# Kernel optimization log

Measured on AMD Instinct MI355X. Metric: run time of the kernel, lower is better.

The kernel has to match this reference:

```python
import jax, jax.numpy as jnp
import numpy as np

B, F, M, N, H, O = 8, 128, 256, 1024, 64, 128
BN_EPS = 1e-5
COS_EPS = 1e-8


def _bn(x, g, b, m, v):
    # inference-mode BatchNorm over channel axis 1
    shape = [1] * x.ndim
    shape[1] = -1
    return g.reshape(shape) * (x - m.reshape(shape)) * jax.lax.rsqrt(v.reshape(shape) + BN_EPS) + b.reshape(shape)


def setup_inputs() -> dict:
    key = jax.random.key(0)
    ks = jax.random.split(key, 24)
    def n(k, shape, s=1.0):
        return jax.random.normal(k, shape, dtype=jnp.float32) * s
    inp = {}
    inp['template_feature'] = n(ks[0], (B, F, M))
    inp['search_feature'] = n(ks[1], (B, F, N))
    # SharedMLP 1x1 conv weights (bias=False because bn=True)
    inp['W1'] = n(ks[2], (H, F + 1), 0.05)
    inp['W2'] = n(ks[3], (H, H), 0.05)
    inp['W3'] = n(ks[4], (H, H), 0.05)
    # fea_layer: conv1d(H, bn=True) then conv1d(O, activation=None, bias=True)
    inp['Wc1'] = n(ks[5], (H, H), 0.05)
    inp['Wc2'] = n(ks[6], (O, H), 0.05)
    inp['bc2'] = n(ks[7], (O,), 0.05)
    for i, nm in enumerate(['1', '2', '3', 'c1']):
        inp['g' + nm] = 1.0 + n(ks[8 + i], (H,), 0.1)
        inp['b' + nm] = n(ks[12 + i], (H,), 0.1)
        inp['m' + nm] = n(ks[16 + i], (H,), 0.01)
        inp['v' + nm] = jax.random.uniform(ks[20 + i], (H,), minval=0.5, maxval=1.5, dtype=jnp.float32)
    return inp


def reference(template_feature, search_feature, W1, W2, W3, Wc1, Wc2, bc2,
              g1, b1, m1, v1, g2, b2, m2, v2, g3, b3, m3, v3, gc1, bc1, mc1, vc1):
    t, s = template_feature, search_feature
    # pairwise cosine similarity over channel dim (no BxFxMxN expand needed)
    dot = jnp.einsum('bfm,bfn->bmn', t, s)
    nt = jnp.linalg.norm(t, axis=1)  # (B, M)
    ns = jnp.linalg.norm(s, axis=1)  # (B, N)
    cos = dot / jnp.maximum(nt[:, :, None] * ns[:, None, :], COS_EPS)  # (B, M, N)
    # first 1x1 conv on concat(cos, expand(t)) computed fused (no concat materialization)
    h = jnp.einsum('hf,bfm->bhm', W1[:, 1:], t)[..., None] + W1[:, 0][None, :, None, None] * cos[:, None]
    h = jax.nn.relu(_bn(h, g1, b1, m1, v1))  # (B, H, M, N)
    h = jax.nn.relu(_bn(jnp.einsum('gh,bhmn->bgmn', W2, h), g2, b2, m2, v2))
    h = jax.nn.relu(_bn(jnp.einsum('gh,bhmn->bgmn', W3, h), g3, b3, m3, v3))
    p = jnp.max(h, axis=2)  # max-pool over M -> (B, H, N)
    c = jax.nn.relu(_bn(jnp.einsum('gh,bhn->bgn', Wc1, p), gc1, bc1, mc1, vc1))
    return jnp.einsum('oh,bhn->bon', Wc2, c) + bc2[None, :, None]  # (B, O, N)
```

## Files before the change

kernel.cpp:

```cpp
#include <hip/hip_runtime.h>


#define BB 8
#define FF 128
#define MM 256
#define NN 1024
#define HH 64
#define OO 128
#define BN_EPS 1e-5f
#define COS_EPS 1e-8f

#define WS_U     0
#define WS_C2    64
#define WS_C3    128
#define WS_CC1   192
#define WS_W2H   256
#define WS_W3H   2304
#define WS_WC1F  8448
#define WS_A1    12544
#define WS_NT    143616
#define WS_NS    145664
#define WS_COSH  153856
#define WS_P     1202432
#define PS       524288

typedef _Float16 half2v __attribute__((ext_vector_type(2)));
typedef _Float16 half4  __attribute__((ext_vector_type(4)));
typedef _Float16 half8  __attribute__((ext_vector_type(8)));
typedef __attribute__((ext_vector_type(4))) float f32x4;

__device__ __forceinline__ unsigned int pkh2(float a, float b){
  auto h = __builtin_amdgcn_cvt_pkrtz(a, b);
  return __builtin_bit_cast(unsigned int, h);
}
__device__ __forceinline__ half2v u2h(unsigned int u){
  return __builtin_bit_cast(half2v, u);
}
__device__ __forceinline__ unsigned int h2u(half2v v){
  return __builtin_bit_cast(unsigned int, v);
}
__device__ __forceinline__ unsigned int relu2(unsigned int d){
  half2v v = __builtin_elementwise_max(u2h(d), (half2v){(_Float16)0, (_Float16)0});
  return h2u(v);
}
__device__ __forceinline__ unsigned int bh1(unsigned int up, half2v c, unsigned int ap){
  half2v v = __builtin_elementwise_fma(u2h(up), c, u2h(ap));
  v = __builtin_elementwise_max(v, (half2v){(_Float16)0, (_Float16)0});
  return h2u(v);
}
__device__ __forceinline__ float dot4(float4 a, float4 b, float acc){
  acc = fmaf(a.x, b.x, acc); acc = fmaf(a.y, b.y, acc);
  acc = fmaf(a.z, b.z, acc); acc = fmaf(a.w, b.w, acc);
  return acc;
}

__global__ __launch_bounds__(256) void k_prep(const float* t_, const float* s_,
    const float* W1, const float* W2, const float* W3, const float* Wc1,
    const float* g1, const float* b1, const float* m1, const float* v1,
    const float* g2, const float* b2, const float* m2, const float* v2,
    const float* g3, const float* b3, const float* m3, const float* v3,
    const float* gc1,const float* bc1,const float* mc1,const float* vc1,
    float* ws){
  __shared__ float W1s[64][133];
  int t = threadIdx.x;
  int bx = blockIdx.x;
  if (bx < 256){
    int b = bx >> 5, m0 = (bx & 31)*8;
    for (int idx = t; idx < 8192; idx += 256){
      int h = idx >> 7, f = idx & 127;
      W1s[h][f] = W1[h*129 + 1 + f];
    }
    __syncthreads();
    int h = t & 63, mg = t >> 6;
    const float* tp = t_ + (size_t)b*FF*MM + m0 + mg*2;
    float acc0 = 0.f, acc1 = 0.f;
    for (int f = 0; f < FF; f++){
      float wv = W1s[h][f];
      float2 tv = *(const float2*)&tp[(size_t)f*MM];
      acc0 = fmaf(wv, tv.x, acc0); acc1 = fmaf(wv, tv.y, acc1);
    }
    float a1 = g1[h] / sqrtf(v1[h] + BN_EPS);
    float c1 = b1[h] - a1*m1[h];
    unsigned short* dst = (unsigned short*)(ws + WS_A1) + ((size_t)(b*MM + m0 + mg*2))*64 + h;
    dst[0]  = (unsigned short)(pkh2(fmaf(a1, acc0, c1), 0.f) & 0xFFFFu);
    dst[64] = (unsigned short)(pkh2(fmaf(a1, acc1, c1), 0.f) & 0xFFFFu);
  } else if (bx < 416){
    __shared__ float red[4][64];
    int x = t & 63, fq = t >> 6;
    int idx = (bx - 256)*64 + x;
    const float* ptr; size_t stride;
    if (idx < BB*MM){
      int b = idx >> 8, m = idx & 255;
      ptr = t_ + (size_t)b*FF*MM + m; stride = MM;
    } else {
      int j = idx - BB*MM;
      int b = j >> 10, n = j & 1023;
      ptr = s_ + (size_t)b*FF*NN + n; stride = NN;
    }
    float acc = 0.f;
    for (int f = fq*32; f < fq*32 + 32; f++){
      float v = ptr[(size_t)f*stride]; acc = fmaf(v, v, acc);
    }
    red[fq][x] = acc;
    __syncthreads();
    if (fq == 0)
      ws[WS_NT + idx] = sqrtf(red[0][x] + red[1][x] + red[2][x] + red[3][x]);
  } else {
    if (t < 64){
      float a1 = g1[t] / sqrtf(v1[t] + BN_EPS);
      ws[WS_U + t]   = a1 * W1[t*129];
      float a2 = g2[t] / sqrtf(v2[t] + BN_EPS);
      ws[WS_C2 + t]  = b2[t] - a2*m2[t];
      float a3 = g3[t] / sqrtf(v3[t] + BN_EPS);
      ws[WS_C3 + t]  = b3[t] - a3*m3[t];
      float ac = gc1[t] / sqrtf(vc1[t] + BN_EPS);
      ws[WS_CC1 + t] = bc1[t] - ac*mc1[t];
    }
    unsigned short* w2h = (unsigned short*)(ws + WS_W2H);
    unsigned short* w3h = (unsigned short*)(ws + WS_W3H);
    for (int i = t; i < 4096; i += 256){
      int g = i >> 6;
      float a2 = g2[g] / sqrtf(v2[g] + BN_EPS);
      w2h[i] = __builtin_bit_cast(unsigned short, (_Float16)(a2 * W2[i]));
      float a3 = g3[g] / sqrtf(v3[g] + BN_EPS);
      w3h[i] = __builtin_bit_cast(unsigned short, (_Float16)(a3 * W3[i]));
      float ac = gc1[g] / sqrtf(vc1[g] + BN_EPS);
      ws[WS_WC1F + i] = ac * Wc1[i];
    }
  }
}

__global__ __launch_bounds__(256) void k_cos(const float* t_, const float* s_, float* ws){
  __shared__ __align__(16) unsigned short tS[64][136];
  __shared__ __align__(16) unsigned short sS[64][136];
  __shared__ float ntS[64], nsS[64];
  int t = threadIdx.x;
  int lane = t & 63, w = t >> 6;
  int ln15 = lane & 15, quad = lane >> 4;
  int m0 = blockIdx.x*64, n0 = blockIdx.y*64, b = blockIdx.z;
  {
    int x = t & 63;
    const float* tb = t_ + (size_t)b*FF*MM + m0 + x;
    const float* sb = s_ + (size_t)b*FF*NN + n0 + x;
    #pragma unroll
    for (int k = 0; k < 16; k++){
      int fp = w*16 + k;
      *(unsigned int*)&tS[x][2*fp] = pkh2(tb[(size_t)(2*fp)*MM], tb[(size_t)(2*fp+1)*MM]);
      *(unsigned int*)&sS[x][2*fp] = pkh2(sb[(size_t)(2*fp)*NN], sb[(size_t)(2*fp+1)*NN]);
    }
    if (t < 64) ntS[t] = ws[WS_NT + b*MM + m0 + t];
    else if (t < 128) nsS[t-64] = ws[WS_NS + b*NN + n0 + (t-64)];
  }
  __syncthreads();
  half8 A4[4];
  #pragma unroll
  for (int kc = 0; kc < 4; kc++)
    A4[kc] = *(const half8*)&sS[w*16 + ln15][kc*32 + quad*8];
  float4 ns4 = *(const float4*)&nsS[w*16 + quad*4];
  int nb = n0 + w*16 + quad*4;
  unsigned short* cosw = (unsigned short*)(ws + WS_COSH);
  #pragma unroll
  for (int mt = 0; mt < 4; mt++){
    f32x4 acc = (f32x4){0.f,0.f,0.f,0.f};
    #pragma unroll
    for (int kc = 0; kc < 4; kc++){
      half8 B4 = *(const half8*)&tS[mt*16 + ln15][kc*32 + quad*8];
      acc = __builtin_amdgcn_mfma_f32_16x16x32_f16(A4[kc], B4, acc, 0, 0, 0);
    }
    int m = m0 + mt*16 + ln15;
    float ntv = ntS[mt*16 + ln15];
    float c0 = acc[0] * __builtin_amdgcn_rcpf(fmaxf(ntv*ns4.x, COS_EPS));
    float c1 = acc[1] * __builtin_amdgcn_rcpf(fmaxf(ntv*ns4.y, COS_EPS));
    float c2 = acc[2] * __builtin_amdgcn_rcpf(fmaxf(ntv*ns4.z, COS_EPS));
    float c3 = acc[3] * __builtin_amdgcn_rcpf(fmaxf(ntv*ns4.w, COS_EPS));
    uint2 vv;
    vv.x = pkh2(c0, c1);
    vv.y = pkh2(c2, c3);
    *(uint2*)&cosw[(size_t)(b*MM + m)*NN + nb] = vv;
  }
}

__global__ __launch_bounds__(256, 3) void k_main(const float* ws, float* Pp){
  __shared__ __align__(16) float redS[3][16][68];
  int t = threadIdx.x;
  int lane = t & 63, w = t >> 6;
  int ln15 = lane & 15, quad = lane >> 4;
  int b = blockIdx.y;
  int n0 = blockIdx.x * 16;
  int ms = blockIdx.z;

  const unsigned short* w2h = (const unsigned short*)(ws + WS_W2H);
  const unsigned short* w3h = (const unsigned short*)(ws + WS_W3H);
  half8 W2A[4][2];
  half4 W3A[4][4];
  f32x4 c2v[4];
  #pragma unroll
  for (int rt = 0; rt < 4; rt++){
    int g = rt*16 + ln15;
    #pragma unroll
    for (int kk = 0; kk < 2; kk++)
      W2A[rt][kk] = *(const half8*)&w2h[g*64 + kk*32 + quad*8];
    #pragma unroll
    for (int ks = 0; ks < 4; ks++)
      W3A[rt][ks] = *(const half4*)&w3h[g*64 + ks*16 + quad*4];
    float4 cb2 = *(const float4*)&ws[WS_C2 + rt*16 + quad*4];
    c2v[rt] = (f32x4){cb2.x, cb2.y, cb2.z, cb2.w};
  }
  f32x4 zf = (f32x4){0.f, 0.f, 0.f, 0.f};
  unsigned int upk[2][4];
  #pragma unroll
  for (int kk = 0; kk < 2; kk++){
    float4 ua = *(const float4*)&ws[WS_U + kk*32 + quad*8];
    float4 ub = *(const float4*)&ws[WS_U + kk*32 + quad*8 + 4];
    upk[kk][0] = pkh2(ua.x, ua.y); upk[kk][1] = pkh2(ua.z, ua.w);
    upk[kk][2] = pkh2(ub.x, ub.y); upk[kk][3] = pkh2(ub.z, ub.w);
  }
  const unsigned short* A1H = (const unsigned short*)(ws + WS_A1) + (size_t)b*MM*64;
  int n = n0 + ln15;
  const unsigned short* cosP = (const unsigned short*)(ws + WS_COSH)
                               + (size_t)b*MM*NN + n;

  f32x4 p[4];
  #pragma unroll
  for (int rt = 0; rt < 4; rt++)
    p[rt] = (f32x4){-3.0e38f, -3.0e38f, -3.0e38f, -3.0e38f};

  int m0i = ms*128 + w;
  unsigned int cu = cosP[(size_t)m0i*NN];
  uint4 a1a = *(const uint4*)&A1H[(size_t)m0i*64 + quad*8];
  uint4 a1b = *(const uint4*)&A1H[(size_t)m0i*64 + 32 + quad*8];

  for (int mc = 0; mc < 32; mc++){
    int mN = ms*128 + (mc < 31 ? mc + 1 : 31)*4 + w;
    unsigned int cuN = cosP[(size_t)mN*NN];
    uint4 a1aN = *(const uint4*)&A1H[(size_t)mN*64 + quad*8];
    uint4 a1bN = *(const uint4*)&A1H[(size_t)mN*64 + 32 + quad*8];

    unsigned int cd = cu | (cu << 16);
    half2v ch = u2h(cd);
    uint4 q0, q1;
    q0.x = bh1(upk[0][0], ch, a1a.x); q0.y = bh1(upk[0][1], ch, a1a.y);
    q0.z = bh1(upk[0][2], ch, a1a.z); q0.w = bh1(upk[0][3], ch, a1a.w);
    q1.x = bh1(upk[1][0], ch, a1b.x); q1.y = bh1(upk[1][1], ch, a1b.y);
    q1.z = bh1(upk[1][2], ch, a1b.z); q1.w = bh1(upk[1][3], ch, a1b.w);
    half8 b0h = __builtin_bit_cast(half8, q0);
    half8 b1h = __builtin_bit_cast(half8, q1);

    f32x4 acc[4];
    #pragma unroll
    for (int rt = 0; rt < 4; rt++){
      acc[rt] = __builtin_amdgcn_mfma_f32_16x16x32_f16(W2A[rt][0], b0h, c2v[rt], 0, 0, 0);
      acc[rt] = __builtin_amdgcn_mfma_f32_16x16x32_f16(W2A[rt][1], b1h, acc[rt], 0, 0, 0);
    }

    half4 pk[4];
    #pragma unroll
    for (int ks = 0; ks < 4; ks++){
      uint2 vv;
      vv.x = relu2(pkh2(acc[ks][0], acc[ks][1]));
      vv.y = relu2(pkh2(acc[ks][2], acc[ks][3]));
      pk[ks] = __builtin_bit_cast(half4, vv);
    }

    #pragma unroll
    for (int rt = 0; rt < 4; rt++){
      f32x4 a3 = __builtin_amdgcn_mfma_f32_16x16x16f16(W3A[rt][0], pk[0], zf, 0, 0, 0);
      a3 = __builtin_amdgcn_mfma_f32_16x16x16f16(W3A[rt][1], pk[1], a3, 0, 0, 0);
      a3 = __builtin_amdgcn_mfma_f32_16x16x16f16(W3A[rt][2], pk[2], a3, 0, 0, 0);
      a3 = __builtin_amdgcn_mfma_f32_16x16x16f16(W3A[rt][3], pk[3], a3, 0, 0, 0);
      #pragma unroll
      for (int r = 0; r < 4; r++) p[rt][r] = fmaxf(p[rt][r], a3[r]);
    }

    cu = cuN; a1a = a1aN; a1b = a1bN;
  }

  __syncthreads();
  if (w >= 1){
    #pragma unroll
    for (int rt = 0; rt < 4; rt++){
      f32x4 v = p[rt];
      *(float4*)&redS[w-1][ln15][rt*16 + quad*4] = make_float4(v[0], v[1], v[2], v[3]);
    }
  }
  __syncthreads();
  if (w == 0){
    float* Pb = Pp + (size_t)ms*PS + ((size_t)(b*NN + n) << 6);
    #pragma unroll
    for (int rt = 0; rt < 4; rt++){
      float4 o1 = *(const float4*)&redS[0][ln15][rt*16 + quad*4];
      float4 o2 = *(const float4*)&redS[1][ln15][rt*16 + quad*4];
      float4 o3 = *(const float4*)&redS[2][ln15][rt*16 + quad*4];
      float4 c3b = *(const float4*)&ws[WS_C3 + rt*16 + quad*4];
      float4 r4;
      r4.x = fmaxf(fmaxf(fmaxf(p[rt][0], o1.x), fmaxf(o2.x, o3.x)) + c3b.x, 0.f);
      r4.y = fmaxf(fmaxf(fmaxf(p[rt][1], o1.y), fmaxf(o2.y, o3.y)) + c3b.y, 0.f);
      r4.z = fmaxf(fmaxf(fmaxf(p[rt][2], o1.z), fmaxf(o2.z, o3.z)) + c3b.z, 0.f);
      r4.w = fmaxf(fmaxf(fmaxf(p[rt][3], o1.w), fmaxf(o2.w, o3.w)) + c3b.w, 0.f);
      *(float4*)&Pb[rt*16 + quad*4] = r4;
    }
  }
}

__global__ __launch_bounds__(256) void k_tail(const float* Wc2, const float* bc2,
                                              const float* ws, float* out){
  __shared__ float WT[64][68];
  __shared__ float pT[32][68];
  __shared__ float cS[32][68];
  int t = threadIdx.x;
  int n0 = blockIdx.x * 32;
  int b = blockIdx.y;
  for (int i = t; i < 4096; i += 256) WT[i >> 6][i & 63] = ws[WS_WC1F + i];
  const float* P0 = ws + WS_P + ((size_t)(b*NN + n0) << 6);
  const float* P1 = P0 + PS;
  for (int i = t; i < 2048; i += 256) pT[i >> 6][i & 63] = fmaxf(P0[i], P1[i]);
  __syncthreads();
  {
    int n = t & 31, q = t >> 5;
    for (int k = 0; k < 8; k++){
      int g = q*8 + k;
      float acc = ws[WS_CC1 + g];
      for (int hs = 0; hs < 64; hs += 4){
        float4 wv = *(const float4*)&WT[g][hs];
        float4 pv = *(const float4*)&pT[n][hs];
        acc = dot4(wv, pv, acc);
      }
      cS[n][g] = fmaxf(acc, 0.f);
    }
  }
  __syncthreads();
  {
    int o = t & 127, hf = t >> 7;
    float bco = bc2[o];
    float accO[16];
    #pragma unroll
    for (int i = 0; i < 16; i++) accO[i] = bco;
    for (int hs = 0; hs < 64; hs += 4){
      float4 w4 = *(const float4*)&Wc2[o*64 + hs];
      #pragma unroll
      for (int i = 0; i < 16; i++){
        float4 cv = *(const float4*)&cS[hf*16 + i][hs];
        accO[i] = dot4(w4, cv, accO[i]);
      }
    }
    #pragma unroll
    for (int i = 0; i < 16; i++)
      out[((size_t)(b*OO + o))*NN + n0 + hf*16 + i] = accO[i];
  }
}

extern "C" void kernel_launch(void* const* d_in, const int* in_sizes, int n_in,
                              void* d_out, int out_size, void* d_ws, size_t ws_size,
                              hipStream_t stream){
  (void)in_sizes; (void)n_in; (void)out_size; (void)ws_size;
  const float* t_  = (const float*)d_in[0];
  const float* s_  = (const float*)d_in[1];
  const float* W1  = (const float*)d_in[2];
  const float* W2  = (const float*)d_in[3];
  const float* W3  = (const float*)d_in[4];
  const float* Wc1 = (const float*)d_in[5];
  const float* Wc2 = (const float*)d_in[6];
  const float* bc2 = (const float*)d_in[7];
  const float* g1 = (const float*)d_in[8],  *b1 = (const float*)d_in[9],
             * m1 = (const float*)d_in[10], *v1 = (const float*)d_in[11];
  const float* g2 = (const float*)d_in[12], *b2 = (const float*)d_in[13],
             * m2 = (const float*)d_in[14], *v2 = (const float*)d_in[15];
  const float* g3 = (const float*)d_in[16], *b3 = (const float*)d_in[17],
             * m3 = (const float*)d_in[18], *v3 = (const float*)d_in[19];
  const float* gc1 = (const float*)d_in[20], *bc1 = (const float*)d_in[21],
             * mc1 = (const float*)d_in[22], *vc1 = (const float*)d_in[23];
  float* ws = (float*)d_ws;
  float* out = (float*)d_out;

  k_prep<<<417, 256, 0, stream>>>(t_, s_, W1, W2, W3, Wc1,
      g1,b1,m1,v1, g2,b2,m2,v2, g3,b3,m3,v3, gc1,bc1,mc1,vc1, ws);
  k_cos<<<dim3(4, 16, 8), 256, 0, stream>>>(t_, s_, ws);
  k_main<<<dim3(64, 8, 2), 256, 0, stream>>>(ws, ws + WS_P);
  k_tail<<<dim3(32, 8), 256, 0, stream>>>(Wc2, bc2, ws, out);
}
```

Before: 178.4 us.

## Use K=32 MFMA for layer 3 and software-pipeline layer 2/3 across M steps

The W3 weights are stored with a column permutation that matches the register layout of the packed layer-2 ReLU output. This lets layer 3 use two 16x16x32 MFMAs per row tile instead of four 16x16x16 ones, with no shuffles. The M loop is also restructured into a two-stage software pipeline: layer 3 for one step runs interleaved with layer 2 of the next, and loads are prefetched two steps ahead with double buffers. This is meant to cut MFMA instruction count and hide dependency latency between the two matmuls, at the cost of more live registers under the 3-wave occupancy bound.

```diff
diff --git a/kernel.cpp b/kernel.cpp
--- a/kernel.cpp
+++ b/kernel.cpp
@@ -25,7 +25,6 @@
 #define PS       524288
 
 typedef _Float16 half2v __attribute__((ext_vector_type(2)));
-typedef _Float16 half4  __attribute__((ext_vector_type(4)));
 typedef _Float16 half8  __attribute__((ext_vector_type(8)));
 typedef __attribute__((ext_vector_type(4))) float f32x4;
 
@@ -119,12 +118,17 @@
     unsigned short* w2h = (unsigned short*)(ws + WS_W2H);
     unsigned short* w3h = (unsigned short*)(ws + WS_W3H);
     for (int i = t; i < 4096; i += 256){
-      int g = i >> 6;
-      float a2 = g2[g] / sqrtf(v2[g] + BN_EPS);
+      int gp = i >> 6;
+      float a2 = g2[gp] / sqrtf(v2[gp] + BN_EPS);
       w2h[i] = __builtin_bit_cast(unsigned short, (_Float16)(a2 * W2[i]));
-      float a3 = g3[g] / sqrtf(v3[g] + BN_EPS);
-      w3h[i] = __builtin_bit_cast(unsigned short, (_Float16)(a3 * W3[i]));
-      float ac = gc1[g] / sqrtf(vc1[g] + BN_EPS);
+      {
+        int s = i & 63;
+        int kk = s >> 5, s2 = s & 31, q = s2 >> 3, j = s2 & 7;
+        int g = kk*32 + ((j < 4) ? (q*4 + j) : (16 + q*4 + (j - 4)));
+        float a3 = g3[gp] / sqrtf(v3[gp] + BN_EPS);
+        w3h[i] = __builtin_bit_cast(unsigned short, (_Float16)(a3 * W3[gp*64 + g]));
+      }
+      float ac = gc1[gp] / sqrtf(vc1[gp] + BN_EPS);
       ws[WS_WC1F + i] = ac * Wc1[i];
     }
   }
@@ -180,6 +184,47 @@
   }
 }
 
+#define K_LD(mi, cu_, aa, ab) { \
+  int mm_ = ms*128 + (((mi) < 32) ? (mi) : 31)*4 + w; \
+  cu_ = cosP[(size_t)mm_*NN]; \
+  aa = *(const uint4*)&A1H[(size_t)mm_*64 + quad*8]; \
+  ab = *(const uint4*)&A1H[(size_t)mm_*64 + 32 + quad*8]; }
+
+#define K_STEP(cu_, aa, ab) { \
+  unsigned int cd_ = (cu_) | ((cu_) << 16); \
+  half2v ch_ = u2h(cd_); \
+  uint4 q0_, q1_; \
+  q0_.x = bh1(upk[0][0], ch_, (aa).x); q0_.y = bh1(upk[0][1], ch_, (aa).y); \
+  q0_.z = bh1(upk[0][2], ch_, (aa).z); q0_.w = bh1(upk[0][3], ch_, (aa).w); \
+  q1_.x = bh1(upk[1][0], ch_, (ab).x); q1_.y = bh1(upk[1][1], ch_, (ab).y); \
+  q1_.z = bh1(upk[1][2], ch_, (ab).z); q1_.w = bh1(upk[1][3], ch_, (ab).w); \
+  half8 b0h_ = __builtin_bit_cast(half8, q0_); \
+  half8 b1h_ = __builtin_bit_cast(half8, q1_); \
+  f32x4 a0_, a1_, a2_, a3x_; \
+  a0_ = __builtin_amdgcn_mfma_f32_16x16x32_f16(W2A[0][0], b0h_, c2v[0], 0, 0, 0); \
+  a0_ = __builtin_amdgcn_mfma_f32_16x16x32_f16(W2A[0][1], b1h_, a0_, 0, 0, 0); \
+  a1_ = __builtin_amdgcn_mfma_f32_16x16x32_f16(W2A[1][0], b0h_, c2v[1], 0, 0, 0); \
+  a1_ = __builtin_amdgcn_mfma_f32_16x16x32_f16(W2A[1][1], b1h_, a1_, 0, 0, 0); \
+  a2_ = __builtin_amdgcn_mfma_f32_16x16x32_f16(W2A[2][0], b0h_, c2v[2], 0, 0, 0); \
+  a2_ = __builtin_amdgcn_mfma_f32_16x16x32_f16(W2A[2][1], b1h_, a2_, 0, 0, 0); \
+  a3x_ = __builtin_amdgcn_mfma_f32_16x16x32_f16(W2A[3][0], b0h_, c2v[3], 0, 0, 0); \
+  a3x_ = __builtin_amdgcn_mfma_f32_16x16x32_f16(W2A[3][1], b1h_, a3x_, 0, 0, 0); \
+  e0P.x = relu2(pkh2(a0_[0], a0_[1])); e0P.y = relu2(pkh2(a0_[2], a0_[3])); \
+  e0P.z = relu2(pkh2(a1_[0], a1_[1])); e0P.w = relu2(pkh2(a1_[2], a1_[3])); \
+  e1P.x = relu2(pkh2(a2_[0], a2_[1])); e1P.y = relu2(pkh2(a2_[2], a2_[3])); \
+  e1P.z = relu2(pkh2(a3x_[0], a3x_[1])); e1P.w = relu2(pkh2(a3x_[2], a3x_[3])); }
+
+#define K_L3 { \
+  half8 pe0_ = __builtin_bit_cast(half8, e0P); \
+  half8 pe1_ = __builtin_bit_cast(half8, e1P); \
+  _Pragma("unroll") \
+  for (int rt = 0; rt < 4; rt++){ \
+    f32x4 a3_ = __builtin_amdgcn_mfma_f32_16x16x32_f16(W3A[rt][0], pe0_, zf, 0, 0, 0); \
+    a3_ = __builtin_amdgcn_mfma_f32_16x16x32_f16(W3A[rt][1], pe1_, a3_, 0, 0, 0); \
+    _Pragma("unroll") \
+    for (int r = 0; r < 4; r++) p[rt][r] = fmaxf(p[rt][r], a3_[r]); \
+  } }
+
 __global__ __launch_bounds__(256, 3) void k_main(const float* ws, float* Pp){
   __shared__ __align__(16) float redS[3][16][68];
   int t = threadIdx.x;
@@ -191,18 +236,16 @@
 
   const unsigned short* w2h = (const unsigned short*)(ws + WS_W2H);
   const unsigned short* w3h = (const unsigned short*)(ws + WS_W3H);
-  half8 W2A[4][2];
-  half4 W3A[4][4];
+  half8 W2A[4][2], W3A[4][2];
   f32x4 c2v[4];
   #pragma unroll
   for (int rt = 0; rt < 4; rt++){
     int g = rt*16 + ln15;
     #pragma unroll
-    for (int kk = 0; kk < 2; kk++)
+    for (int kk = 0; kk < 2; kk++){
       W2A[rt][kk] = *(const half8*)&w2h[g*64 + kk*32 + quad*8];
-    #pragma unroll
-    for (int ks = 0; ks < 4; ks++)
-      W3A[rt][ks] = *(const half4*)&w3h[g*64 + ks*16 + quad*4];
+      W3A[rt][kk] = *(const half8*)&w3h[g*64 + kk*32 + quad*8];
+    }
     float4 cb2 = *(const float4*)&ws[WS_C2 + rt*16 + quad*4];
     c2v[rt] = (f32x4){cb2.x, cb2.y, cb2.z, cb2.w};
   }
@@ -225,55 +268,29 @@
   for (int rt = 0; rt < 4; rt++)
     p[rt] = (f32x4){-3.0e38f, -3.0e38f, -3.0e38f, -3.0e38f};
 
-  int m0i = ms*128 + w;
-  unsigned int cu = cosP[(size_t)m0i*NN];
-  uint4 a1a = *(const uint4*)&A1H[(size_t)m0i*64 + quad*8];
-  uint4 a1b = *(const uint4*)&A1H[(size_t)m0i*64 + 32 + quad*8];
-
-  for (int mc = 0; mc < 32; mc++){
-    int mN = ms*128 + (mc < 31 ? mc + 1 : 31)*4 + w;
-    unsigned int cuN = cosP[(size_t)mN*NN];
-    uint4 a1aN = *(const uint4*)&A1H[(size_t)mN*64 + quad*8];
-    uint4 a1bN = *(const uint4*)&A1H[(size_t)mN*64 + 32 + quad*8];
-
-    unsigned int cd = cu | (cu << 16);
-    half2v ch = u2h(cd);
-    uint4 q0, q1;
-    q0.x = bh1(upk[0][0], ch, a1a.x); q0.y = bh1(upk[0][1], ch, a1a.y);
-    q0.z = bh1(upk[0][2], ch, a1a.z); q0.w = bh1(upk[0][3], ch, a1a.w);
-    q1.x = bh1(upk[1][0], ch, a1b.x); q1.y = bh1(upk[1][1], ch, a1b.y);
-    q1.z = bh1(upk[1][2], ch, a1b.z); q1.w = bh1(upk[1][3], ch, a1b.w);
-    half8 b0h = __builtin_bit_cast(half8, q0);
-    half8 b1h = __builtin_bit_cast(half8, q1);
-
-    f32x4 acc[4];
-    #pragma unroll
-    for (int rt = 0; rt < 4; rt++){
-      acc[rt] = __builtin_amdgcn_mfma_f32_16x16x32_f16(W2A[rt][0], b0h, c2v[rt], 0, 0, 0);
-      acc[rt] = __builtin_amdgcn_mfma_f32_16x16x32_f16(W2A[rt][1], b1h, acc[rt], 0, 0, 0);
-    }
-
-    half4 pk[4];
-    #pragma unroll
-    for (int ks = 0; ks < 4; ks++){
-      uint2 vv;
-      vv.x = relu2(pkh2(acc[ks][0], acc[ks][1]));
-      vv.y = relu2(pkh2(acc[ks][2], acc[ks][3]));
-      pk[ks] = __builtin_bit_cast(half4, vv);
-    }
-
-    #pragma unroll
-    for (int rt = 0; rt < 4; rt++){
-      f32x4 a3 = __builtin_amdgcn_mfma_f32_16x16x16f16(W3A[rt][0], pk[0], zf, 0, 0, 0);
-      a3 = __builtin_amdgcn_mfma_f32_16x16x16f16(W3A[rt][1], pk[1], a3, 0, 0, 0);
-      a3 = __builtin_amdgcn_mfma_f32_16x16x16f16(W3A[rt][2], pk[2], a3, 0, 0, 0);
-      a3 = __builtin_amdgcn_mfma_f32_16x16x16f16(W3A[rt][3], pk[3], a3, 0, 0, 0);
-      #pragma unroll
-      for (int r = 0; r < 4; r++) p[rt][r] = fmaxf(p[rt][r], a3[r]);
-    }
-
-    cu = cuN; a1a = a1aN; a1b = a1bN;
-  }
+  uint4 e0P, e1P;
+
+  unsigned int cuA, cuB;
+  uint4 a1aA, a1bA, a1aB, a1bB;
+
+  K_LD(0, cuA, a1aA, a1bA)
+  K_LD(1, cuB, a1aB, a1bB)
+
+  K_STEP(cuA, a1aA, a1bA)
+  K_LD(2, cuA, a1aA, a1bA)
+
+  for (int k = 0; k < 15; k++){
+    K_L3
+    K_STEP(cuB, a1aB, a1bB)
+    K_LD(2*k + 3, cuB, a1aB, a1bB)
+    K_L3
+    K_STEP(cuA, a1aA, a1bA)
+    K_LD(2*k + 4, cuA, a1aA, a1bA)
+  }
+
+  K_L3
+  K_STEP(cuB, a1aB, a1bB)
+  K_L3
 
   __syncthreads();
   if (w >= 1){
```

Result: faster. 169.6 us (-4.9%).
